# Optimization experiments

Hardware: AMD Instinct MI355X
Metric: run time of the kernel (lower is better)

## Reference

```python
import jax, jax.numpy as jnp
import numpy as np
from jax import lax

B, T, H_IN, W_IN = 16, 100, 159, 132   # T = n_frames (channels AND time steps)
HID = 100                               # lstm_h
NC, NL = 14, 3                          # num_classes, num_locations
FEAT = (H_IN - 27) * W_IN               # 17424, GRU input size


def setup_inputs() -> dict:
    key = jax.random.key(0)
    ks = jax.random.split(key, 16)
    s = 0.05
    return {
        "x":    jax.random.normal(ks[0], (B, T, H_IN, W_IN), jnp.float32),
        "w1":   jax.random.normal(ks[1], (T, T, 10, 1), jnp.float32) * s,
        "bc1":  jax.random.normal(ks[2], (T,), jnp.float32) * s,
        "w2":   jax.random.normal(ks[3], (T, T, 10, 1), jnp.float32) * s,
        "bc2":  jax.random.normal(ks[4], (T,), jnp.float32) * s,
        "w3":   jax.random.normal(ks[5], (T, T, 10, 1), jnp.float32) * s,
        "bc3":  jax.random.normal(ks[6], (T,), jnp.float32) * s,
        "w_ih": jax.random.normal(ks[7], (3 * HID, FEAT), jnp.float32) * 0.01,
        "w_hh": jax.random.normal(ks[8], (3 * HID, HID), jnp.float32) * s,
        "b_ih": jax.random.normal(ks[9], (3 * HID,), jnp.float32) * s,
        "b_hh": jax.random.normal(ks[10], (3 * HID,), jnp.float32) * s,
        "w_y1": jax.random.normal(ks[11], (NC, HID), jnp.float32) * s,
        "b_y1": jax.random.normal(ks[12], (NC,), jnp.float32) * s,
        "w_y2": jax.random.normal(ks[13], (NL, HID), jnp.float32) * s,
        "b_y2": jax.random.normal(ks[14], (NL,), jnp.float32) * s,
    }


def _conv(x, w, b):
    y = lax.conv_general_dilated(x, w, (1, 1), 'VALID',
                                 dimension_numbers=('NCHW', 'OIHW', 'NCHW'))
    return y + b[None, :, None, None]


def _gru(gi, w_ih, w_hh, b_ih, b_hh):
    # gi: [B, T, FEAT] batch_first; torch GRU gate order r, z, n
    xw = jnp.einsum('btf,gf->btg', gi, w_ih) + b_ih        # [B,T,3H]
    h0 = jnp.zeros((gi.shape[0], HID), gi.dtype)

    def step(h, xw_t):
        gh = h @ w_hh.T + b_hh                             # [B,3H]
        r = jax.nn.sigmoid(xw_t[:, :HID] + gh[:, :HID])
        z = jax.nn.sigmoid(xw_t[:, HID:2 * HID] + gh[:, HID:2 * HID])
        n = jnp.tanh(xw_t[:, 2 * HID:] + r * gh[:, 2 * HID:])
        h_new = (1.0 - z) * n + z * h
        return h_new, h_new

    _, hs = lax.scan(step, h0, jnp.swapaxes(xw, 0, 1))     # [T,B,H]
    return jnp.swapaxes(hs, 0, 1)                          # [B,T,H]


def reference(x, w1, bc1, w2, bc2, w3, bc3,
              w_ih, w_hh, b_ih, b_hh, w_y1, b_y1, w_y2, b_y2):
    c = _conv(_conv(_conv(x, w1, bc1), w2, bc2), w3, bc3)  # [B,T,H3,W]
    gi = c.reshape(c.shape[0], c.shape[1], -1)             # [B,T,FEAT]
    g = _gru(gi, w_ih, w_hh, b_ih, b_hh)                   # [B,T,HID]
    y1 = jax.nn.sigmoid(jnp.einsum('bth,ch->btc', g, w_y1) + b_y1)
    y2 = jnp.tanh(jnp.einsum('bth,ch->btc', g, w_y2) + b_y2) * 10.0
    return (y1, y2)
```

## Files before the change

kernel.cpp:

```cpp
#include <hip/hip_runtime.h>
#include <math.h>

#define TDIM  100
#define HIDN  100
#define G3    300
#define WD    132
#define CIP   104
#define KP    1056
#define NKC   33
#define GIK   17440
#define GIN   320
#define BTOT  16
#define INP0  (159 * WD)

typedef float    f32x4 __attribute__((ext_vector_type(4)));
typedef _Float16 f16x8 __attribute__((ext_vector_type(8)));
typedef _Float16 f16x4 __attribute__((ext_vector_type(4)));

static __device__ __forceinline__ float sigmoidf_(float x) {
    return 1.f / (1.f + __expf(-x));
}
static __device__ __forceinline__ float tanhf_(float x) {
    const float e = __expf(-2.f * fabsf(x));
    const float t = (1.f - e) / (1.f + e);
    return copysignf(t, x);
}
static __device__ __forceinline__ float bcastf(float v, int l) {
    return __int_as_float(__builtin_amdgcn_readlane(__float_as_int(v), l));
}

static __device__ __forceinline__ void gl16(const _Float16* g, _Float16* l)
{
    __builtin_amdgcn_global_load_lds(
        (const __attribute__((address_space(1))) void*)g,
        (__attribute__((address_space(3))) void*)l,
        16, 0, 0);
}

static __device__ __forceinline__ int xcd_remap_lin()
{
    const int nwg = gridDim.x * gridDim.y * gridDim.z;
    const int lin = (blockIdx.z * gridDim.y + blockIdx.y) * gridDim.x + blockIdx.x;
    const int q = nwg >> 3, r = nwg & 7;
    const int xcd = lin & 7, idx = lin >> 3;
    return (xcd < r ? xcd * (q + 1) : r * (q + 1) + (xcd - r) * q) + idx;
}

__global__ __launch_bounds__(256)
void prep_convw(const float* __restrict__ w, _Float16* __restrict__ wp)
{
    const int idx = blockIdx.x * 256 + threadIdx.x;
    if (idx >= 128 * KP) return;
    const int co = idx / KP, k = idx - co * KP;
    const int kh = k / CIP, ci = k - kh * CIP;
    float v = 0.f;
    if (co < 100 && ci < 100 && kh < 10)
        v = w[(co * 100 + ci) * 10 + kh];
    wp[idx] = (_Float16)v;
}

__global__ __launch_bounds__(256)
void prep_wih(const float* __restrict__ w_ih, _Float16* __restrict__ wihp)
{
    const int k = blockIdx.x * 256 + threadIdx.x;
    const int n = blockIdx.y;
    if (k >= GIK) return;
    const float v = (n < G3 && k < 17424) ? w_ih[(size_t)n * 17424 + k] : 0.f;
    wihp[(size_t)n * GIK + k] = (_Float16)v;
}

__global__ __launch_bounds__(256)
void transpose_x(const float* __restrict__ x, _Float16* __restrict__ xT)
{
    __shared__ __align__(16) _Float16 t[64][116];
    const int tid = threadIdx.x;
    const int p0  = blockIdx.x * 64;
    const int b   = blockIdx.y;
    const int pl  = tid & 63;
    const int p   = p0 + pl;
    t[tid >> 2][100 + (tid & 3)] = (_Float16)0.f;
    const float* xb = x + (size_t)b * 100 * INP0;
    #pragma unroll
    for (int i = 0; i < 25; ++i) {
        const int ci = (tid >> 6) + i * 4;
        const float v = (p < INP0) ? xb[(size_t)ci * INP0 + p] : 0.f;
        t[pl][ci] = (_Float16)v;
    }
    __syncthreads();
    _Float16* xTb = xT + (size_t)b * INP0 * CIP;
    #pragma unroll
    for (int i = 0; i < 7; ++i) {
        const int idx = tid + i * 256;
        if (idx < 64 * 26) {
            const int rr = idx / 26;
            const int c  = (idx - rr * 26) * 4;
            if (p0 + rr < INP0)
                *(f16x4*)(xTb + (size_t)(p0 + rr) * CIP + c) = *(const f16x4*)&t[rr][c];
        }
    }
}

template<int HIN, bool OUTT>
__global__ __launch_bounds__(256)
void conv_mfma(const _Float16* __restrict__ actT,
               const _Float16* __restrict__ wp,
               const float*    __restrict__ bias,
               _Float16* __restrict__ out)
{
    constexpr int HOUT = HIN - 9;
    constexpr int NP   = HOUT * WD;
    constexpr int INP  = HIN * WD;

    __shared__ __align__(16) _Float16 As[3][128][32];
    __shared__ __align__(16) _Float16 Bs[3][128][32];

    const int tid  = threadIdx.x;
    const int work = xcd_remap_lin();
    const int p0   = (work % gridDim.x) * 128;
    const int b    = work / gridDim.x;
    const _Float16* act_b = actT + (size_t)b * INP * CIP;

    const int wv = tid >> 6;
    const int l  = tid & 63;
    const int ln = tid & 15;
    const int lq = (tid & 63) >> 4;
    const int rl  = l >> 2;
    const int run = l & 3;

    const _Float16* srcA0 = wp + (size_t)(wv * 16 + rl) * KP + run * 8;
    const _Float16* srcA1 = wp + (size_t)(64 + wv * 16 + rl) * KP + run * 8;
    const int plB0 = wv * 32 + rl;
    const int plB1 = wv * 32 + 16 + rl;

    f32x4 acc[7][2] = {};

    auto stage = [&](int buf, int kk) {
        const int k0 = kk * 32;
        gl16(srcA0 + k0, &As[buf][wv * 16][0]);
        gl16(srcA1 + k0, &As[buf][64 + wv * 16][0]);
        const int k   = k0 + run * 8;
        const int kh  = k / CIP;
        const int ci0 = k - kh * CIP;
        const int row0 = min(p0 + plB0 + kh * WD, INP - 1);
        const int row1 = min(p0 + plB1 + kh * WD, INP - 1);
        gl16(act_b + (size_t)row0 * CIP + ci0, &Bs[buf][wv * 32][0]);
        gl16(act_b + (size_t)row1 * CIP + ci0, &Bs[buf][wv * 32 + 16][0]);
    };

    stage(0, 0);
    stage(1, 1);
    int rb = 0;
    for (int kk = 0; kk < NKC; ++kk) {
        if (kk + 1 < NKC) {
            asm volatile("s_waitcnt vmcnt(4) lgkmcnt(0)\n\ts_barrier" ::: "memory");
        } else {
            asm volatile("s_waitcnt vmcnt(0) lgkmcnt(0)\n\ts_barrier" ::: "memory");
        }
        if (kk + 2 < NKC) {
            int sb = rb + 2; if (sb >= 3) sb -= 3;
            stage(sb, kk + 2);
        }
        const f16x8 bf0 = *(const f16x8*)&Bs[rb][(wv * 2 + 0) * 16 + ln][lq * 8];
        const f16x8 bf1 = *(const f16x8*)&Bs[rb][(wv * 2 + 1) * 16 + ln][lq * 8];
        #pragma unroll
        for (int mt = 0; mt < 7; ++mt) {
            const f16x8 af = *(const f16x8*)&As[rb][mt * 16 + ln][lq * 8];
            acc[mt][0] = __builtin_amdgcn_mfma_f32_16x16x32_f16(af, bf0, acc[mt][0], 0, 0, 0);
            acc[mt][1] = __builtin_amdgcn_mfma_f32_16x16x32_f16(af, bf1, acc[mt][1], 0, 0, 0);
        }
        rb = (rb + 1 == 3) ? 0 : rb + 1;
    }

    #pragma unroll
    for (int j = 0; j < 2; ++j) {
        const int p = p0 + (wv * 2 + j) * 16 + ln;
        if (p >= NP) continue;
        if (OUTT) {
            _Float16* orow = out + (size_t)b * NP * CIP + (size_t)p * CIP;
            #pragma unroll
            for (int mt = 0; mt < 7; ++mt) {
                const int co0 = mt * 16 + lq * 4;
                if (co0 < CIP) {
                    f16x4 v;
                    #pragma unroll
                    for (int r = 0; r < 4; ++r) {
                        const int co = co0 + r;
                        v[r] = (_Float16)(acc[mt][j][r] + (co < 100 ? bias[co] : 0.f));
                    }
                    *(f16x4*)(orow + co0) = v;
                }
            }
        } else {
            #pragma unroll
            for (int mt = 0; mt < 7; ++mt) {
                #pragma unroll
                for (int r = 0; r < 4; ++r) {
                    const int co = mt * 16 + lq * 4 + r;
                    if (co < 100)
                        out[((size_t)b * 100 + co) * GIK + p] =
                            (_Float16)(acc[mt][j][r] + bias[co]);
                }
            }
        }
    }
}

__global__ __launch_bounds__(256)
void gemm_mfma(const _Float16* __restrict__ A,
               const _Float16* __restrict__ B,
               float* __restrict__ C)
{
    constexpr int NKG = GIK / 32;
    constexpr int SEG = 69;
    __shared__ __align__(16) _Float16 As[2][128][32];
    __shared__ __align__(16) _Float16 Bs[2][64][32];

    const int tid  = threadIdx.x;
    const int work = xcd_remap_lin();
    const int bx   = work % 5;
    const int rem  = work / 5;
    const int by   = rem % 13;
    const int bz   = rem / 13;

    const int n0  = bx * 64;
    const int m0  = by * 128;
    const int k00 = bz * SEG;
    const int k01 = min(NKG, k00 + SEG);

    const int wv = tid >> 6, ln = tid & 15, lq = (tid & 63) >> 4;
    const int l  = tid & 63;
    const int rl = l >> 2, run = l & 3;

    const _Float16* srcA0 = A + (size_t)(m0 + wv * 32 + rl) * GIK + run * 8;
    const _Float16* srcA1 = A + (size_t)(m0 + wv * 32 + 16 + rl) * GIK + run * 8;
    const _Float16* srcB  = B + (size_t)(n0 + wv * 16 + rl) * GIK + run * 8;

    f32x4 acc[2][4] = {};

    auto stage = [&](int buf, int kk) {
        const int k0 = kk * 32;
        gl16(srcA0 + k0, &As[buf][wv * 32][0]);
        gl16(srcA1 + k0, &As[buf][wv * 32 + 16][0]);
        gl16(srcB  + k0, &Bs[buf][wv * 16][0]);
    };

    stage(0, k00);
    int cur = 0;
    for (int kk = k00; kk < k01; ++kk) {
        if (kk + 1 < k01) {
            stage(cur ^ 1, kk + 1);
            asm volatile("s_waitcnt vmcnt(3)\n\ts_barrier" ::: "memory");
        } else {
            asm volatile("s_waitcnt vmcnt(0)\n\ts_barrier" ::: "memory");
        }
        const f16x8 af0 = *(const f16x8*)&As[cur][wv * 32 + ln][lq * 8];
        const f16x8 af1 = *(const f16x8*)&As[cur][wv * 32 + 16 + ln][lq * 8];
        #pragma unroll
        for (int nt = 0; nt < 4; ++nt) {
            const f16x8 bf = *(const f16x8*)&Bs[cur][nt * 16 + ln][lq * 8];
            acc[0][nt] = __builtin_amdgcn_mfma_f32_16x16x32_f16(af0, bf, acc[0][nt], 0, 0, 0);
            acc[1][nt] = __builtin_amdgcn_mfma_f32_16x16x32_f16(af1, bf, acc[1][nt], 0, 0, 0);
        }
        asm volatile("s_waitcnt lgkmcnt(0)\n\ts_barrier" ::: "memory");
        cur ^= 1;
    }
    #pragma unroll
    for (int mt = 0; mt < 2; ++mt) {
        #pragma unroll
        for (int nt = 0; nt < 4; ++nt) {
            const int n = n0 + nt * 16 + ln;
            const int m = m0 + wv * 32 + mt * 16 + lq * 4;
            if (n < G3) {
                #pragma unroll
                for (int rr = 0; rr < 4; ++rr)
                    if (m + rr < 1600)
                        atomicAdd(&C[(size_t)(m + rr) * G3 + n], acc[mt][nt][rr]);
            }
        }
    }
}

__global__ __launch_bounds__(256)
void init_xw_k(const float* __restrict__ b_ih, float* __restrict__ xw)
{
    const int i = blockIdx.x * 256 + threadIdx.x;
    if (i < BTOT * TDIM * G3) xw[i] = b_ih[i % G3];
}

__global__ __launch_bounds__(640)
void gru3_k(const float* __restrict__ xw, const float* __restrict__ w_hh,
            const float* __restrict__ b_hh, float* __restrict__ gout)
{
    __shared__ float h_s[128];
    __shared__ float ghp[2][304];

    const int tid  = threadIdx.x;
    const int b    = blockIdx.x;
    const int wave = tid >> 6;
    const int lane = tid & 63;
    const int half = (wave >= 5) ? 1 : 0;
    const int row  = (half ? wave - 5 : wave) * 64 + lane;
    const bool act = (row < G3);

    float wreg[50];
    #pragma unroll
    for (int j = 0; j < 50; ++j)
        wreg[j] = act ? w_hh[row * HIDN + half * 50 + j] : 0.f;
    const float bh = (act && half == 0) ? b_hh[row] : 0.f;

    if (tid < 128) h_s[tid] = 0.f;
    __syncthreads();

    const bool gate = (tid < HIDN);
    const float* xwb = xw + (size_t)b * TDIM * G3;

    float xA0 = 0.f, xA1 = 0.f, xA2 = 0.f;
    float xB0 = 0.f, xB1 = 0.f, xB2 = 0.f;
    if (gate) {
        xA0 = xwb[tid];
        xA1 = xwb[HIDN + tid];
        xA2 = xwb[2 * HIDN + tid];
    }

    auto matvec = [&]() {
        const float hlo = h_s[lane];
        const float hhi = h_s[64 + lane];
        float acc = bh;
        if (half == 0) {
            #pragma unroll
            for (int k = 0; k < 50; ++k)
                acc += wreg[k] * bcastf(hlo, k);
        } else {
            #pragma unroll
            for (int k = 0; k < 14; ++k)
                acc += wreg[k] * bcastf(hlo, 50 + k);
            #pragma unroll
            for (int k = 14; k < 50; ++k)
                acc += wreg[k] * bcastf(hhi, k - 14);
        }
        if (act) ghp[half][row] = acc;
    };

    auto gates = [&](int t, float x0, float x1, float x2) {
        if (gate) {
            const float g0 = ghp[0][tid]            + ghp[1][tid];
            const float g1 = ghp[0][HIDN + tid]     + ghp[1][HIDN + tid];
            const float g2 = ghp[0][2 * HIDN + tid] + ghp[1][2 * HIDN + tid];
            const float hp = h_s[tid];
            const float r  = sigmoidf_(x0 + g0);
            const float z  = sigmoidf_(x1 + g1);
            const float n  = tanhf_(x2 + r * g2);
            const float hn = (1.f - z) * n + z * hp;
            h_s[tid] = hn;
            gout[((size_t)b * TDIM + t) * HIDN + tid] = hn;
        }
    };

    for (int t = 0; t < TDIM; t += 2) {
        if (gate && t + 1 < TDIM) {
            const float* p = xwb + (size_t)(t + 1) * G3;
            xB0 = p[tid]; xB1 = p[HIDN + tid]; xB2 = p[2 * HIDN + tid];
        }
        matvec();
        __syncthreads();
        gates(t, xA0, xA1, xA2);
        __syncthreads();

        if (gate && t + 2 < TDIM) {
            const float* p = xwb + (size_t)(t + 2) * G3;
            xA0 = p[tid]; xA1 = p[HIDN + tid]; xA2 = p[2 * HIDN + tid];
        }
        matvec();
        __syncthreads();
        gates(t + 1, xB0, xB1, xB2);
        __syncthreads();
    }
}

__global__ __launch_bounds__(256)
void heads_k(const float* __restrict__ g,
             const float* __restrict__ wy1, const float* __restrict__ by1,
             const float* __restrict__ wy2, const float* __restrict__ by2,
             float* __restrict__ out)
{
    constexpr int NY1 = BTOT * TDIM * 14;
    constexpr int NY2 = BTOT * TDIM * 3;
    const int idx = blockIdx.x * 256 + threadIdx.x;
    if (idx < NY1) {
        const int row = idx / 14, c = idx - row * 14;
        const float* gr = g + (size_t)row * HIDN;
        const float* wr = wy1 + c * HIDN;
        float acc = by1[c];
        for (int k = 0; k < HIDN; ++k) acc += gr[k] * wr[k];
        out[idx] = sigmoidf_(acc);
    } else if (idx < NY1 + NY2) {
        const int j = idx - NY1;
        const int row = j / 3, c = j - row * 3;
        const float* gr = g + (size_t)row * HIDN;
        const float* wr = wy2 + c * HIDN;
        float acc = by2[c];
        for (int k = 0; k < HIDN; ++k) acc += gr[k] * wr[k];
        out[NY1 + row * 3 + c] = tanhf(acc) * 10.f;
    }
}

extern "C" void kernel_launch(void* const* d_in, const int* in_sizes, int n_in,
                              void* d_out, int out_size, void* d_ws, size_t ws_size,
                              hipStream_t stream)
{
    (void)in_sizes; (void)n_in; (void)out_size; (void)ws_size;
    const float* x    = (const float*)d_in[0];
    const float* w1   = (const float*)d_in[1];
    const float* bc1  = (const float*)d_in[2];
    const float* w2   = (const float*)d_in[3];
    const float* bc2  = (const float*)d_in[4];
    const float* w3   = (const float*)d_in[5];
    const float* bc3  = (const float*)d_in[6];
    const float* w_ih = (const float*)d_in[7];
    const float* w_hh = (const float*)d_in[8];
    const float* b_ih = (const float*)d_in[9];
    const float* b_hh = (const float*)d_in[10];
    const float* wy1  = (const float*)d_in[11];
    const float* by1  = (const float*)d_in[12];
    const float* wy2  = (const float*)d_in[13];
    const float* by2  = (const float*)d_in[14];
    float* out = (float*)d_out;

    char* wsp = (char*)d_ws;
    auto alloc = [&](size_t bytes) -> char* {
        char* p = wsp; wsp += (bytes + 255) & ~(size_t)255; return p;
    };
    _Float16* wp1  = (_Float16*)alloc((size_t)128 * KP * 2);
    _Float16* wp2  = (_Float16*)alloc((size_t)128 * KP * 2);
    _Float16* wp3  = (_Float16*)alloc((size_t)128 * KP * 2);
    float*    xw   = (float*)   alloc((size_t)BTOT * TDIM * G3 * 4);
    float*    g    = (float*)   alloc((size_t)BTOT * TDIM * HIDN * 4);
    char*     regA = alloc((size_t)BTOT * INP0 * CIP * 2);
    char*     regB = alloc((size_t)BTOT * 150 * WD * CIP * 2);

    _Float16* xT   = (_Float16*)regA;
    _Float16* c2T  = (_Float16*)regA;
    _Float16* wihp = (_Float16*)regA;
    _Float16* c1T  = (_Float16*)regB;
    _Float16* gi   = (_Float16*)regB;

    prep_convw<<<(128 * KP + 255) / 256, 256, 0, stream>>>(w1, wp1);
    prep_convw<<<(128 * KP + 255) / 256, 256, 0, stream>>>(w2, wp2);
    prep_convw<<<(128 * KP + 255) / 256, 256, 0, stream>>>(w3, wp3);
    init_xw_k<<<(BTOT * TDIM * G3 + 255) / 256, 256, 0, stream>>>(b_ih, xw);

    transpose_x<<<dim3((INP0 + 63) / 64, BTOT), 256, 0, stream>>>(x, xT);
    conv_mfma<159, true ><<<dim3(155, BTOT), 256, 0, stream>>>(xT,  wp1, bc1, c1T);
    conv_mfma<150, true ><<<dim3(146, BTOT), 256, 0, stream>>>(c1T, wp2, bc2, c2T);
    conv_mfma<141, false><<<dim3(137, BTOT), 256, 0, stream>>>(c2T, wp3, bc3, gi);

    prep_wih<<<dim3((GIK + 255) / 256, GIN), 256, 0, stream>>>(w_ih, wihp);
    gemm_mfma<<<dim3(5, 13, 8), 256, 0, stream>>>(gi, wihp, xw);
    gru3_k<<<16, 640, 0, stream>>>(xw, w_hh, b_hh, g);
    heads_k<<<(27200 + 255) / 256, 256, 0, stream>>>(g, wy1, by1, wy2, by2, out);
}
```

Before: 871.2 us.

## Fold three linear convolutions into one composed 28-tap convolution

Since the three (10x1) convolutions have no nonlinearity between them, the weights are composed on device into a single 28-tap kernel with a combined bias. One MFMA conv over the raw input then replaces the three conv passes and their intermediate activation round-trips. The K dimension grows to 2912 (91 chunks) while the number of output tiles matches the last conv. This cuts total MACs and memory traffic, but adds small prep kernels and may change fp16 rounding behaviour.

Result: slower. 1.049 ms (+20.4%).

```diff
diff --git a/kernel.cpp b/kernel.cpp
--- a/kernel.cpp
+++ b/kernel.cpp
@@ -6,12 +6,13 @@
 #define G3    300
 #define WD    132
 #define CIP   104
-#define KP    1056
-#define NKC   33
+#define KP3   2912
+#define NKC3  91
 #define GIK   17440
 #define GIN   320
 #define BTOT  16
 #define INP0  (159 * WD)
+#define NPF   17424
 
 typedef float    f32x4 __attribute__((ext_vector_type(4)));
 typedef _Float16 f16x8 __attribute__((ext_vector_type(8)));
@@ -47,16 +48,103 @@
 }
 
 __global__ __launch_bounds__(256)
-void prep_convw(const float* __restrict__ w, _Float16* __restrict__ wp)
+void prep_w12(const float* __restrict__ w1, const float* __restrict__ w2,
+              float* __restrict__ w12)
 {
     const int idx = blockIdx.x * 256 + threadIdx.x;
-    if (idx >= 128 * KP) return;
-    const int co = idx / KP, k = idx - co * KP;
-    const int kh = k / CIP, ci = k - kh * CIP;
-    float v = 0.f;
-    if (co < 100 && ci < 100 && kh < 10)
-        v = w[(co * 100 + ci) * 10 + kh];
-    wp[idx] = (_Float16)v;
+    if (idx >= 10000) return;
+    const int a = idx / 100, c = idx - a * 100;
+    float acc[19];
+    #pragma unroll
+    for (int k = 0; k < 19; ++k) acc[k] = 0.f;
+    for (int b = 0; b < 100; ++b) {
+        float v1[10], v2[10];
+        #pragma unroll
+        for (int k = 0; k < 10; ++k) v1[k] = w1[((size_t)b * 100 + c) * 10 + k];
+        #pragma unroll
+        for (int k = 0; k < 10; ++k) v2[k] = w2[((size_t)a * 100 + b) * 10 + k];
+        #pragma unroll
+        for (int k2 = 0; k2 < 10; ++k2)
+            #pragma unroll
+            for (int k1 = 0; k1 < 10; ++k1)
+                acc[k1 + k2] += v2[k2] * v1[k1];
+    }
+    #pragma unroll
+    for (int k = 0; k < 19; ++k) w12[(size_t)idx * 19 + k] = acc[k];
+}
+
+__global__ __launch_bounds__(256)
+void zero_wp(_Float16* __restrict__ wp)
+{
+    const int idx = blockIdx.x * 256 + threadIdx.x;
+    if (idx < 128 * KP3) wp[idx] = (_Float16)0.f;
+}
+
+__global__ __launch_bounds__(256)
+void prep_w123(const float* __restrict__ w12, const float* __restrict__ w3,
+               _Float16* __restrict__ wp)
+{
+    const int idx = blockIdx.x * 256 + threadIdx.x;
+    if (idx >= 10000) return;
+    const int o = idx / 100, c = idx - o * 100;
+    float acc[28];
+    #pragma unroll
+    for (int k = 0; k < 28; ++k) acc[k] = 0.f;
+    for (int a = 0; a < 100; ++a) {
+        float v3[10], v12[19];
+        #pragma unroll
+        for (int k = 0; k < 10; ++k) v3[k] = w3[((size_t)o * 100 + a) * 10 + k];
+        #pragma unroll
+        for (int k = 0; k < 19; ++k) v12[k] = w12[((size_t)a * 100 + c) * 19 + k];
+        #pragma unroll
+        for (int k3 = 0; k3 < 10; ++k3)
+            #pragma unroll
+            for (int k12 = 0; k12 < 19; ++k12)
+                acc[k3 + k12] += v3[k3] * v12[k12];
+    }
+    #pragma unroll
+    for (int kh = 0; kh < 28; ++kh)
+        wp[(size_t)o * KP3 + kh * CIP + c] = (_Float16)acc[kh];
+}
+
+__global__ __launch_bounds__(128)
+void prep_bias(const float* __restrict__ w2, const float* __restrict__ w3,
+               const float* __restrict__ bc1, const float* __restrict__ bc2,
+               const float* __restrict__ bc3, float* __restrict__ bias123)
+{
+    __shared__ float b12[100];
+    const int tid = threadIdx.x;
+    if (tid < 100) {
+        float acc = bc2[tid];
+        for (int o = 0; o < 100; ++o) {
+            float s = 0.f;
+            #pragma unroll
+            for (int k = 0; k < 10; ++k) s += w2[((size_t)tid * 100 + o) * 10 + k];
+            acc += s * bc1[o];
+        }
+        b12[tid] = acc;
+    }
+    __syncthreads();
+    if (tid < 100) {
+        float acc = bc3[tid];
+        for (int a = 0; a < 100; ++a) {
+            float s = 0.f;
+            #pragma unroll
+            for (int k = 0; k < 10; ++k) s += w3[((size_t)tid * 100 + a) * 10 + k];
+            acc += s * b12[a];
+        }
+        bias123[tid] = acc;
+    }
+}
+
+__global__ __launch_bounds__(256)
+void zero_gipad(_Float16* __restrict__ gi)
+{
+    const int idx = blockIdx.x * 256 + threadIdx.x;
+    if (idx < 1600 * 16) {
+        const int row = idx >> 4, col = NPF + (idx & 15);
+        gi[(size_t)row * GIK + col] = (_Float16)0.f;
+    }
 }
 
 __global__ __launch_bounds__(256)
@@ -100,17 +188,13 @@
     }
 }
 
-template<int HIN, bool OUTT>
-__global__ __launch_bounds__(256)
-void conv_mfma(const _Float16* __restrict__ actT,
-               const _Float16* __restrict__ wp,
-               const float*    __restrict__ bias,
-               _Float16* __restrict__ out)
-{
-    constexpr int HOUT = HIN - 9;
-    constexpr int NP   = HOUT * WD;
-    constexpr int INP  = HIN * WD;
-
+__global__ __launch_bounds__(256)
+void convF(const _Float16* __restrict__ actT,
+           const _Float16* __restrict__ wp,
+           const float*    __restrict__ bias,
+           _Float16* __restrict__ out)
+{
+    constexpr int INP = INP0;
     __shared__ __align__(16) _Float16 As[3][128][32];
     __shared__ __align__(16) _Float16 Bs[3][128][32];
 
@@ -127,8 +211,8 @@
     const int rl  = l >> 2;
     const int run = l & 3;
 
-    const _Float16* srcA0 = wp + (size_t)(wv * 16 + rl) * KP + run * 8;
-    const _Float16* srcA1 = wp + (size_t)(64 + wv * 16 + rl) * KP + run * 8;
+    const _Float16* srcA0 = wp + (size_t)(wv * 16 + rl) * KP3 + run * 8;
+    const _Float16* srcA1 = wp + (size_t)(64 + wv * 16 + rl) * KP3 + run * 8;
     const int plB0 = wv * 32 + rl;
     const int plB1 = wv * 32 + 16 + rl;
 
@@ -150,13 +234,13 @@
     stage(0, 0);
     stage(1, 1);
     int rb = 0;
-    for (int kk = 0; kk < NKC; ++kk) {
-        if (kk + 1 < NKC) {
+    for (int kk = 0; kk < NKC3; ++kk) {
+        if (kk + 1 < NKC3) {
             asm volatile("s_waitcnt vmcnt(4) lgkmcnt(0)\n\ts_barrier" ::: "memory");
         } else {
             asm volatile("s_waitcnt vmcnt(0) lgkmcnt(0)\n\ts_barrier" ::: "memory");
         }
-        if (kk + 2 < NKC) {
+        if (kk + 2 < NKC3) {
             int sb = rb + 2; if (sb >= 3) sb -= 3;
             stage(sb, kk + 2);
         }
@@ -174,32 +258,15 @@
     #pragma unroll
     for (int j = 0; j < 2; ++j) {
         const int p = p0 + (wv * 2 + j) * 16 + ln;
-        if (p >= NP) continue;
-        if (OUTT) {
-            _Float16* orow = out + (size_t)b * NP * CIP + (size_t)p * CIP;
-            #pragma unroll
-            for (int mt = 0; mt < 7; ++mt) {
-                const int co0 = mt * 16 + lq * 4;
-                if (co0 < CIP) {
-                    f16x4 v;
-                    #pragma unroll
-                    for (int r = 0; r < 4; ++r) {
-                        const int co = co0 + r;
-                        v[r] = (_Float16)(acc[mt][j][r] + (co < 100 ? bias[co] : 0.f));
-                    }
-                    *(f16x4*)(orow + co0) = v;
-                }
-            }
-        } else {
-            #pragma unroll
-            for (int mt = 0; mt < 7; ++mt) {
-                #pragma unroll
-                for (int r = 0; r < 4; ++r) {
-                    const int co = mt * 16 + lq * 4 + r;
-                    if (co < 100)
-                        out[((size_t)b * 100 + co) * GIK + p] =
-                            (_Float16)(acc[mt][j][r] + bias[co]);
-                }
+        if (p >= NPF) continue;
+        #pragma unroll
+        for (int mt = 0; mt < 7; ++mt) {
+            #pragma unroll
+            for (int r = 0; r < 4; ++r) {
+                const int co = mt * 16 + lq * 4 + r;
+                if (co < 100)
+                    out[((size_t)b * 100 + co) * GIK + p] =
+                        (_Float16)(acc[mt][j][r] + bias[co]);
             }
         }
     }
@@ -430,29 +497,26 @@
     auto alloc = [&](size_t bytes) -> char* {
         char* p = wsp; wsp += (bytes + 255) & ~(size_t)255; return p;
     };
-    _Float16* wp1  = (_Float16*)alloc((size_t)128 * KP * 2);
-    _Float16* wp2  = (_Float16*)alloc((size_t)128 * KP * 2);
-    _Float16* wp3  = (_Float16*)alloc((size_t)128 * KP * 2);
+    _Float16* wp3  = (_Float16*)alloc((size_t)128 * KP3 * 2);
+    float*    w12  = (float*)   alloc((size_t)10000 * 19 * 4);
+    float*    b123 = (float*)   alloc(512);
     float*    xw   = (float*)   alloc((size_t)BTOT * TDIM * G3 * 4);
     float*    g    = (float*)   alloc((size_t)BTOT * TDIM * HIDN * 4);
+    _Float16* gi   = (_Float16*)alloc((size_t)1664 * GIK * 2);
     char*     regA = alloc((size_t)BTOT * INP0 * CIP * 2);
-    char*     regB = alloc((size_t)BTOT * 150 * WD * CIP * 2);
 
     _Float16* xT   = (_Float16*)regA;
-    _Float16* c2T  = (_Float16*)regA;
     _Float16* wihp = (_Float16*)regA;
-    _Float16* c1T  = (_Float16*)regB;
-    _Float16* gi   = (_Float16*)regB;
-
-    prep_convw<<<(128 * KP + 255) / 256, 256, 0, stream>>>(w1, wp1);
-    prep_convw<<<(128 * KP + 255) / 256, 256, 0, stream>>>(w2, wp2);
-    prep_convw<<<(128 * KP + 255) / 256, 256, 0, stream>>>(w3, wp3);
+
+    prep_w12<<<40, 256, 0, stream>>>(w1, w2, w12);
+    zero_wp<<<(128 * KP3 + 255) / 256, 256, 0, stream>>>(wp3);
+    prep_w123<<<40, 256, 0, stream>>>(w12, w3, wp3);
+    prep_bias<<<1, 128, 0, stream>>>(w2, w3, bc1, bc2, bc3, b123);
     init_xw_k<<<(BTOT * TDIM * G3 + 255) / 256, 256, 0, stream>>>(b_ih, xw);
 
     transpose_x<<<dim3((INP0 + 63) / 64, BTOT), 256, 0, stream>>>(x, xT);
-    conv_mfma<159, true ><<<dim3(155, BTOT), 256, 0, stream>>>(xT,  wp1, bc1, c1T);
-    conv_mfma<150, true ><<<dim3(146, BTOT), 256, 0, stream>>>(c1T, wp2, bc2, c2T);
-    conv_mfma<141, false><<<dim3(137, BTOT), 256, 0, stream>>>(c2T, wp3, bc3, gi);
+    convF<<<dim3(137, BTOT), 256, 0, stream>>>(xT, wp3, b123, gi);
+    zero_gipad<<<100, 256, 0, stream>>>(gi);
 
     prep_wih<<<dim3((GIK + 255) / 256, GIN), 256, 0, stream>>>(w_ih, wihp);
     gemm_mfma<<<dim3(5, 13, 8), 256, 0, stream>>>(gi, wihp, xw);
```
